# Optimization experiments

Hardware: AMD Instinct MI355X
Metric: run time of the kernel (lower is better)

Reference implementation:

```python
import jax, jax.numpy as jnp
import numpy as np

N_NODES = 50000
N_EDGES = 800000
B = 512
DIM_IN = 128
D2 = 200
D3 = 200
GC1 = 100
DG = 20
DH = 64
H1 = 128
H2 = 32
BN_EPS = 1e-5


def _lin_init(k, fan_in, fan_out):
    s = 1.0 / np.sqrt(fan_in)
    kw, kb = jax.random.split(k)
    W = jax.random.uniform(kw, (fan_in, fan_out), jnp.float32, -s, s)
    b = jax.random.uniform(kb, (fan_out,), jnp.float32, -s, s)
    return W, b


def setup_inputs() -> dict:
    key = jax.random.key(0)
    ks = jax.random.split(key, 16)
    feat = jax.random.normal(ks[0], (N_NODES, DIM_IN), jnp.float32)
    desc_2d = jax.random.normal(ks[1], (B, D2), jnp.float32)
    desc_3d = jax.random.normal(ks[2], (B, D3), jnp.float32)
    src = jax.random.randint(ks[3], (N_EDGES,), 0, N_NODES, jnp.int32)
    dst = jax.random.randint(ks[4], (N_EDGES,), 0, N_NODES, jnp.int32)
    graph_id = jnp.sort(jax.random.randint(ks[5], (N_NODES,), 0, B, jnp.int32))
    gc1_W, gc1_b = _lin_init(ks[6], DIM_IN, GC1)
    gc2_W, gc2_b = _lin_init(ks[7], GC1, DG)
    pg_W, pg_b = _lin_init(ks[8], DG, DH)
    p2_W, p2_b = _lin_init(ks[9], D2, DH)
    # xavier_uniform for W2
    lim = np.sqrt(6.0 / (DH + DH))
    W2 = jax.random.uniform(ks[10], (DH, DH), jnp.float32, -lim, lim)
    fusion_dim = (DG + 1) * (D2 + 1)
    fc1_W, fc1_b = _lin_init(ks[11], fusion_dim, H1)
    fc2_W, fc2_b = _lin_init(ks[12], H1, H2)
    fc3_W, fc3_b = _lin_init(ks[13], H2, 1)
    return {
        'feat': feat, 'desc_2d': desc_2d, 'desc_3d': desc_3d,
        'gc1_W': gc1_W, 'gc1_b': gc1_b, 'gc2_W': gc2_W, 'gc2_b': gc2_b,
        'pg_W': pg_W, 'pg_b': pg_b, 'p2_W': p2_W, 'p2_b': p2_b, 'W2': W2,
        'fc1_W': fc1_W, 'fc1_b': fc1_b, 'fc2_W': fc2_W, 'fc2_b': fc2_b,
        'fc3_W': fc3_W, 'fc3_b': fc3_b,
        'bn1_g': jnp.ones((H1,), jnp.float32), 'bn1_b': jnp.zeros((H1,), jnp.float32),
        'bn2_g': jnp.ones((H2,), jnp.float32), 'bn2_b': jnp.zeros((H2,), jnp.float32),
        'src': src, 'dst': dst, 'graph_id': graph_id,
    }


def _gcn(h, src, dst, W, b):
    # copy_u -> mean over incoming mailbox -> linear apply
    agg = jax.ops.segment_sum(h[src], dst, num_segments=N_NODES)
    deg = jax.ops.segment_sum(jnp.ones((src.shape[0],), h.dtype), dst, num_segments=N_NODES)
    h_mean = agg / jnp.maximum(deg, 1.0)[:, None]  # zero in-degree -> 0 (DGL default)
    return h_mean @ W + b


def _bn(x, g, b):
    mu = x.mean(0)
    var = x.var(0)
    return (x - mu) * jax.lax.rsqrt(var + BN_EPS) * g + b


def reference(feat, desc_2d, desc_3d, gc1_W, gc1_b, gc2_W, gc2_b,
              pg_W, pg_b, p2_W, p2_b, W2,
              fc1_W, fc1_b, fc2_W, fc2_b, fc3_W, fc3_b,
              bn1_g, bn1_b, bn2_g, bn2_b, src, dst, graph_id):
    h = jax.nn.relu(_gcn(feat, src, dst, gc1_W, gc1_b))          # [N, 100]
    h = jax.nn.relu(_gcn(h, src, dst, gc2_W, gc2_b))             # [N, 20]
    # dgl.mean_nodes: per-graph mean of node features
    cnt = jax.ops.segment_sum(jnp.ones((N_NODES,), h.dtype), graph_id, num_segments=B)
    hg = jax.ops.segment_sum(h, graph_id, num_segments=B) / jnp.maximum(cnt, 1.0)[:, None]  # [B, 20]
    h_g = hg @ pg_W + pg_b                                        # [B, 64]
    h_d = desc_2d @ p2_W + p2_b                                   # [B, 64]
    s = ((h_g @ W2) * h_d).sum(-1)                                # [B]
    a = jax.nn.sigmoid(s)[:, None]                                # [B, 1]
    ones = jnp.ones((B, 1), hg.dtype)
    hg1 = jnp.concatenate([hg, ones], axis=1)                     # [B, 21]
    d1 = jnp.concatenate([a * desc_2d, ones], axis=1)             # [B, 201]
    fusion = (hg1[:, :, None] * d1[:, None, :]).reshape(B, -1)    # [B, 21*201]
    out = jax.nn.relu(_bn(fusion @ fc1_W + fc1_b, bn1_g, bn1_b))
    out = jax.nn.relu(_bn(out @ fc2_W + fc2_b, bn2_g, bn2_b))
    return out @ fc3_W + fc3_b                                    # [B, 1]
```

## Files before the change

### kernel.cpp

```cpp
#include <hip/hip_runtime.h>

#define NN 50000
#define NE 800000
#define NB 512
#define DIN 128
#define DD2 200
#define C1 100
#define C2 20
#define DHH 64
#define HH1 128
#define HH2 32
#define KD 201
#define KDP 204
#define NU 2688
#define SCB 196
#define NCT 7
#define NTILE 3125
#define GB1 782
#define FPB 3125
#define FCB 672
#define PS1 128
#define SLOT 64
#define OVFCAP 8192

typedef short sh8 __attribute__((ext_vector_type(8)));
typedef float f32x4 __attribute__((ext_vector_type(4)));

__device__ __forceinline__ unsigned short f2bf(float x) {
    unsigned u = __float_as_uint(x);
    unsigned r = (u + 0x7fffu + ((u >> 16) & 1u)) >> 16;
    return (unsigned short)r;
}
__device__ __forceinline__ float bf_lo(unsigned u) { return __uint_as_float(u << 16); }
__device__ __forceinline__ float bf_hi(unsigned u) { return __uint_as_float(u & 0xffff0000u); }

__global__ void k_packB_init(const float* __restrict__ W, unsigned short* __restrict__ Bf,
                             int* __restrict__ cnt, float* __restrict__ hgs,
                             int* __restrict__ ovfc) {
    int idx = blockIdx.x * 256 + threadIdx.x;
    if (idx < NCT * 4 * 64) {
        int lane = idx & 63;
        int kc = (idx >> 6) & 3;
        int ct = idx >> 8;
        int col = ct * 16 + (lane & 15);
        int k0 = kc * 32 + (lane >> 4) * 8;
        unsigned short* outp = Bf + (size_t)idx * 8;
        #pragma unroll
        for (int e = 0; e < 8; ++e) {
            float v = (col < C1) ? W[(k0 + e) * C1 + col] : 0.f;
            outp[e] = f2bf(v);
        }
    }
    if (idx < NN) cnt[idx] = 0;
    if (idx < NB * C2) hgs[idx] = 0.f;
    if (idx == 0) *ovfc = 0;
}

__global__ __launch_bounds__(256) void k_front(const float* __restrict__ feat,
                                               const unsigned short* __restrict__ Bf,
                                               unsigned char* __restrict__ t1f8,
                                               const int* __restrict__ dst,
                                               int* __restrict__ cnt,
                                               int* __restrict__ pos,
                                               const float* __restrict__ desc2d,
                                               const float* __restrict__ W1,
                                               float* __restrict__ V) {
    __shared__ float smem[7168];
    const int tid = threadIdx.x;

    if (blockIdx.x >= GB1 && blockIdx.x < GB1 + FPB) {
        int e = (blockIdx.x - GB1) * 256 + tid;
        if (e < NE) pos[e] = atomicAdd(&cnt[dst[e]], 1);
        return;
    }

    if (blockIdx.x < GB1) {
        sh8* sB = (sh8*)smem;
        {
            const uint4* srcp = (const uint4*)Bf;
            uint4* dstp = (uint4*)smem;
            for (int i = tid; i < NCT * 4 * 64; i += 256) dstp[i] = srcp[i];
        }
        __syncthreads();
        const int w = tid >> 6, lane = tid & 63;
        const int ri = lane & 15;
        const int kg = lane >> 4;
        int tile = blockIdx.x * 4 + w;
        if (tile < NTILE) {
            const int n = tile * 16 + ri;
            f32x4 acc[NCT];
            #pragma unroll
            for (int ct = 0; ct < NCT; ++ct) acc[ct] = (f32x4){0.f, 0.f, 0.f, 0.f};
            #pragma unroll
            for (int kc = 0; kc < 4; ++kc) {
                const float* ap = feat + (size_t)n * DIN + kc * 32 + kg * 8;
                float4 a0 = *(const float4*)ap;
                float4 a1 = *(const float4*)(ap + 4);
                union { sh8 v; unsigned short u[8]; } af;
                af.u[0] = f2bf(a0.x); af.u[1] = f2bf(a0.y);
                af.u[2] = f2bf(a0.z); af.u[3] = f2bf(a0.w);
                af.u[4] = f2bf(a1.x); af.u[5] = f2bf(a1.y);
                af.u[6] = f2bf(a1.z); af.u[7] = f2bf(a1.w);
                #pragma unroll
                for (int ct = 0; ct < NCT; ++ct)
                    acc[ct] = __builtin_amdgcn_mfma_f32_16x16x32_bf16(
                        af.v, sB[(ct * 4 + kc) * 64 + lane], acc[ct], 0, 0, 0);
            }
            const int rbase = tile * 16 + kg * 4;
            #pragma unroll
            for (int ct = 0; ct < NCT; ++ct) {
                int col = ct * 16 + ri;
                if (col < C1) {
                    #pragma unroll
                    for (int r = 0; r < 4; ++r) {
                        int pk = __builtin_amdgcn_cvt_pk_fp8_f32(acc[ct][r], acc[ct][r], 0, false);
                        t1f8[(size_t)(rbase + r) * PS1 + col] = (unsigned char)(pk & 0xFF);
                    }
                }
            }
        }
        return;
    }

    {
        float (*S)[KDP] = (float(*)[KDP])smem;
        int fid = blockIdx.x - GB1 - FPB;
        const int i = fid / 32;
        const int rem = fid % 32;
        const int bt = rem >> 1;
        const int half = rem & 1;
        for (int idx = tid; idx < 32 * 50; idx += 256) {
            int r = idx / 50, c4 = idx % 50;
            *(float4*)&S[r][c4 * 4] =
                *(const float4*)(desc2d + (size_t)(bt * 32 + r) * DD2 + c4 * 4);
        }
        __syncthreads();
        const int c = tid & 31;
        const int rg = tid >> 5;
        float acc[4][2];
        #pragma unroll
        for (int r = 0; r < 4; ++r) { acc[r][0] = 0.f; acc[r][1] = 0.f; }
        const float* Wb = W1 + (size_t)i * (KD * HH1) + half * 64 + c;
        for (int k = 0; k < 200; k += 4) {
            const float* Wk = Wb + (size_t)k * HH1;
            float w0[2], w1[2], w2[2], w3[2];
            #pragma unroll
            for (int m = 0; m < 2; ++m) {
                w0[m] = Wk[32 * m];
                w1[m] = Wk[HH1 + 32 * m];
                w2[m] = Wk[2 * HH1 + 32 * m];
                w3[m] = Wk[3 * HH1 + 32 * m];
            }
            #pragma unroll
            for (int r = 0; r < 4; ++r) {
                float4 a4 = *(const float4*)&S[rg * 4 + r][k];
                #pragma unroll
                for (int m = 0; m < 2; ++m)
                    acc[r][m] += a4.x * w0[m] + a4.y * w1[m] + a4.z * w2[m] + a4.w * w3[m];
            }
        }
        #pragma unroll
        for (int r = 0; r < 4; ++r) {
            int b = bt * 32 + rg * 4 + r;
            float* Vr = V + (size_t)b * NU + i * HH1 + half * 64 + c;
            Vr[0] = acc[r][0];
            Vr[32] = acc[r][1];
        }
    }
}

__global__ void k_scat(const int* __restrict__ src, const int* __restrict__ dst,
                       const int* __restrict__ pos, int* __restrict__ epad,
                       int2* __restrict__ ovf, int* __restrict__ ovfc) {
    int e = blockIdx.x * 256 + threadIdx.x;
    if (e < NE) {
        int d = dst[e], p = pos[e], s = src[e];
        if (p < SLOT) {
            epad[(size_t)d * SLOT + p] = s;
        } else {
            int o = atomicAdd(ovfc, 1);
            if (o < OVFCAP) ovf[o] = make_int2(d, s);
        }
    }
}

__global__ __launch_bounds__(256) void k_agg1(const unsigned char* __restrict__ t1f8,
                                              const int* __restrict__ cnt,
                                              const int* __restrict__ epad,
                                              const int2* __restrict__ ovf,
                                              const int* __restrict__ ovfc,
                                              const float* __restrict__ b1,
                                              unsigned* __restrict__ h1b) {
    const int tid = threadIdx.x;
    const int w = tid >> 6, l = tid & 63;
    const int n = blockIdx.x * 4 + w;
    if (n >= NN || l >= 50) return;
    const int deg = cnt[n];
    const int m = deg < SLOT ? deg : SLOT;
    const int* ep = epad + (size_t)n * SLOT;
    const int co = 2 * l;
    float acc0 = 0.f, acc1 = 0.f;
    int e = 0;
    for (; e + 7 < m; e += 8) {
        int s0 = ep[e],     s1 = ep[e + 1], s2 = ep[e + 2], s3 = ep[e + 3];
        int s4 = ep[e + 4], s5 = ep[e + 5], s6 = ep[e + 6], s7 = ep[e + 7];
        int u0 = *(const unsigned short*)(t1f8 + (size_t)s0 * PS1 + co);
        int u1 = *(const unsigned short*)(t1f8 + (size_t)s1 * PS1 + co);
        int u2 = *(const unsigned short*)(t1f8 + (size_t)s2 * PS1 + co);
        int u3 = *(const unsigned short*)(t1f8 + (size_t)s3 * PS1 + co);
        int u4 = *(const unsigned short*)(t1f8 + (size_t)s4 * PS1 + co);
        int u5 = *(const unsigned short*)(t1f8 + (size_t)s5 * PS1 + co);
        int u6 = *(const unsigned short*)(t1f8 + (size_t)s6 * PS1 + co);
        int u7 = *(const unsigned short*)(t1f8 + (size_t)s7 * PS1 + co);
        acc0 += __builtin_amdgcn_cvt_f32_fp8(u0, 0); acc1 += __builtin_amdgcn_cvt_f32_fp8(u0, 1);
        acc0 += __builtin_amdgcn_cvt_f32_fp8(u1, 0); acc1 += __builtin_amdgcn_cvt_f32_fp8(u1, 1);
        acc0 += __builtin_amdgcn_cvt_f32_fp8(u2, 0); acc1 += __builtin_amdgcn_cvt_f32_fp8(u2, 1);
        acc0 += __builtin_amdgcn_cvt_f32_fp8(u3, 0); acc1 += __builtin_amdgcn_cvt_f32_fp8(u3, 1);
        acc0 += __builtin_amdgcn_cvt_f32_fp8(u4, 0); acc1 += __builtin_amdgcn_cvt_f32_fp8(u4, 1);
        acc0 += __builtin_amdgcn_cvt_f32_fp8(u5, 0); acc1 += __builtin_amdgcn_cvt_f32_fp8(u5, 1);
        acc0 += __builtin_amdgcn_cvt_f32_fp8(u6, 0); acc1 += __builtin_amdgcn_cvt_f32_fp8(u6, 1);
        acc0 += __builtin_amdgcn_cvt_f32_fp8(u7, 0); acc1 += __builtin_amdgcn_cvt_f32_fp8(u7, 1);
    }
    for (; e < m; ++e) {
        int u = *(const unsigned short*)(t1f8 + (size_t)ep[e] * PS1 + co);
        acc0 += __builtin_amdgcn_cvt_f32_fp8(u, 0);
        acc1 += __builtin_amdgcn_cvt_f32_fp8(u, 1);
    }
    if (deg > SLOT) {
        int novf = *ovfc; novf = novf < OVFCAP ? novf : OVFCAP;
        for (int j2 = 0; j2 < novf; ++j2) {
            int2 p = ovf[j2];
            if (p.x == n) {
                int u = *(const unsigned short*)(t1f8 + (size_t)p.y * PS1 + co);
                acc0 += __builtin_amdgcn_cvt_f32_fp8(u, 0);
                acc1 += __builtin_amdgcn_cvt_f32_fp8(u, 1);
            }
        }
    }
    float d = (float)(deg > 0 ? deg : 1);
    float v0 = fmaxf(acc0 / d + b1[co], 0.f);
    float v1 = fmaxf(acc1 / d + b1[co + 1], 0.f);
    h1b[(size_t)n * 50 + l] = (unsigned)f2bf(v0) | ((unsigned)f2bf(v1) << 16);
}

__global__ void k_gemm2(const unsigned* __restrict__ h1b, const float* __restrict__ W,
                        unsigned* __restrict__ t2b) {
    __shared__ float sW[C1 * C2];
    __shared__ float sr[16][C1];
    __shared__ float sc[16][C2];
    for (int idx = threadIdx.x; idx < C1 * C2; idx += 320) sW[idx] = W[idx];
    int ln = threadIdx.x / C2, j = threadIdx.x % C2;
    int n0 = blockIdx.x * 16;
    for (int idx = threadIdx.x; idx < 16 * 50; idx += 320) {
        int r = idx / 50, c = idx % 50;
        int n = n0 + r;
        unsigned u = (n < NN) ? h1b[(size_t)n * 50 + c] : 0u;
        sr[r][2 * c] = bf_lo(u);
        sr[r][2 * c + 1] = bf_hi(u);
    }
    __syncthreads();
    if (ln < 16) {
        float acc = 0.f;
        #pragma unroll 4
        for (int k = 0; k < C1; ++k) acc += sr[ln][k] * sW[k * C2 + j];
        sc[ln][j] = acc;
    }
    __syncthreads();
    for (int idx = threadIdx.x; idx < 16 * 10; idx += 320) {
        int r = idx / 10, jp = idx % 10;
        int n = n0 + r;
        if (n < NN)
            t2b[(size_t)n * 10 + jp] =
                (unsigned)f2bf(sc[r][2 * jp]) | ((unsigned)f2bf(sc[r][2 * jp + 1]) << 16);
    }
}

__global__ void k_agg2p(const unsigned* __restrict__ t2b, const int* __restrict__ cnt,
                        const int* __restrict__ epad, const int2* __restrict__ ovf,
                        const int* __restrict__ ovfc, const float* __restrict__ bias,
                        const int* __restrict__ gid, float* __restrict__ hgs) {
    int ln = threadIdx.x / C2, c = threadIdx.x % C2;
    if (ln >= 12) return;
    int n = blockIdx.x * 12 + ln;
    if (n >= NN) return;
    const int deg = cnt[n];
    const int m = deg < SLOT ? deg : SLOT;
    const int* ep = epad + (size_t)n * SLOT;
    const int jp = c >> 1, hi = c & 1;
    float acc = 0.f;
    int e = 0;
    for (; e + 3 < m; e += 4) {
        int s0 = ep[e], s1 = ep[e + 1], s2 = ep[e + 2], s3 = ep[e + 3];
        unsigned u0 = t2b[(size_t)s0 * 10 + jp];
        unsigned u1 = t2b[(size_t)s1 * 10 + jp];
        unsigned u2 = t2b[(size_t)s2 * 10 + jp];
        unsigned u3 = t2b[(size_t)s3 * 10 + jp];
        acc += hi ? bf_hi(u0) : bf_lo(u0);
        acc += hi ? bf_hi(u1) : bf_lo(u1);
        acc += hi ? bf_hi(u2) : bf_lo(u2);
        acc += hi ? bf_hi(u3) : bf_lo(u3);
    }
    for (; e < m; ++e) {
        unsigned u = t2b[(size_t)ep[e] * 10 + jp];
        acc += hi ? bf_hi(u) : bf_lo(u);
    }
    if (deg > SLOT) {
        int novf = *ovfc; novf = novf < OVFCAP ? novf : OVFCAP;
        for (int j2 = 0; j2 < novf; ++j2) {
            int2 p = ovf[j2];
            if (p.x == n) {
                unsigned u = t2b[(size_t)p.y * 10 + jp];
                acc += hi ? bf_hi(u) : bf_lo(u);
            }
        }
    }
    float d = (float)(deg > 0 ? deg : 1);
    float v = acc / d + bias[c];
    v = v > 0.f ? v : 0.f;
    atomicAdd(&hgs[gid[n] * C2 + c], v);
}

__global__ __launch_bounds__(128) void k_hfc1(const float* __restrict__ hgs,
                                              const int* __restrict__ gid,
                                              const float* __restrict__ desc2d,
                                              const float* __restrict__ pgW,
                                              const float* __restrict__ pgb,
                                              const float* __restrict__ p2W,
                                              const float* __restrict__ p2b,
                                              const float* __restrict__ W2,
                                              const float* __restrict__ V,
                                              const float* __restrict__ W1,
                                              float* __restrict__ o1) {
    __shared__ float shg[C2];
    __shared__ float sg[DHH];
    __shared__ float sa;
    const int b = blockIdx.x, tid = threadIdx.x;
    if (tid < C2) {
        int lo = 0, hi = NN;
        while (lo < hi) { int m = (lo + hi) >> 1; if (gid[m] < b) lo = m + 1; else hi = m; }
        int lo2 = lo, hi2 = NN;
        while (lo2 < hi2) { int m = (lo2 + hi2) >> 1; if (gid[m] < b + 1) lo2 = m + 1; else hi2 = m; }
        float dcnt = (float)(lo2 - lo);
        if (dcnt < 1.f) dcnt = 1.f;
        shg[tid] = hgs[b * C2 + tid] / dcnt;
    }
    __syncthreads();
    float hdj = 0.f;
    if (tid < DHH) {
        float hgj = pgb[tid];
        #pragma unroll
        for (int k = 0; k < C2; ++k) hgj += shg[k] * pgW[k * DHH + tid];
        hdj = p2b[tid];
        #pragma unroll 4
        for (int k = 0; k < DD2; ++k) hdj += desc2d[b * DD2 + k] * p2W[k * DHH + tid];
        sg[tid] = hgj;
    }
    __syncthreads();
    if (tid < DHH) {
        float tj = 0.f;
        #pragma unroll 4
        for (int k = 0; k < DHH; ++k) tj += sg[k] * W2[k * DHH + tid];
        float v = tj * hdj;
        #pragma unroll
        for (int off = 32; off; off >>= 1) v += __shfl_xor(v, off, 64);
        if (tid == 0) sa = 1.f / (1.f + expf(-v));
    }
    __syncthreads();
    const int j = tid;
    const float* Vb = V + (size_t)b * NU + j;
    const float* WL = W1 + (size_t)200 * HH1 + j;
    float sv = Vb[20 * HH1];
    float sw = WL[(size_t)20 * KD * HH1];
    #pragma unroll
    for (int i = 0; i < 20; ++i) {
        float h = shg[i];
        sv += h * Vb[i * HH1];
        sw += h * WL[(size_t)i * KD * HH1];
    }
    o1[b * HH1 + j] = sa * sv + sw;
}

__global__ __launch_bounds__(128) void k_fc2s(const float* __restrict__ o1,
                                              const float* __restrict__ g,
                                              const float* __restrict__ beta,
                                              const float* __restrict__ W,
                                              float* __restrict__ o2) {
    __shared__ float r[HH1];
    __shared__ float part[4][HH2];
    const int tid = threadIdx.x;
    float s = 0.f, s2 = 0.f;
    for (int b = 0; b < NB; ++b) {
        float v = o1[b * HH1 + tid];
        s += v; s2 += v * v;
    }
    float mu = s / NB;
    float rstd = rsqrtf(s2 / NB - mu * mu + 1e-5f);
    float scale = rstd * g[tid];
    float shift = beta[tid] - mu * scale;
    const int m = tid & 31, p = tid >> 5;
    for (int q = 0; q < 4; ++q) {
        int b = blockIdx.x * 4 + q;
        float v = o1[b * HH1 + tid];
        __syncthreads();
        r[tid] = fmaxf(v * scale + shift, 0.f);
        __syncthreads();
        float acc = 0.f;
        #pragma unroll 4
        for (int j = p * 32; j < p * 32 + 32; ++j) acc += r[j] * W[j * HH2 + m];
        part[p][m] = acc;
        __syncthreads();
        if (tid < HH2) o2[b * HH2 + tid] = part[0][tid] + part[1][tid] + part[2][tid] + part[3][tid];
    }
}

__global__ __launch_bounds__(512) void k_finals(const float* __restrict__ o2,
                                                const float* __restrict__ g,
                                                const float* __restrict__ beta,
                                                const float* __restrict__ W3,
                                                const float* __restrict__ b3,
                                                float* __restrict__ out) {
    __shared__ float ps[16][HH2], ps2[16][HH2];
    __shared__ float sscale[HH2], sshift[HH2];
    const int tid = threadIdx.x;
    const int gq = tid >> 5, m = tid & 31;
    float s = 0.f, s2 = 0.f;
    for (int rr = 0; rr < 32; ++rr) {
        float v = o2[(gq * 32 + rr) * HH2 + m];
        s += v; s2 += v * v;
    }
    ps[gq][m] = s; ps2[gq][m] = s2;
    __syncthreads();
    if (tid < HH2) {
        float ts = 0.f, ts2 = 0.f;
        #pragma unroll
        for (int q = 0; q < 16; ++q) { ts += ps[q][tid]; ts2 += ps2[q][tid]; }
        float mu = ts / NB;
        float rstd = rsqrtf(ts2 / NB - mu * mu + 1e-5f);
        float scale = rstd * g[tid];
        sscale[tid] = scale;
        sshift[tid] = beta[tid] - mu * scale;
    }
    __syncthreads();
    float acc = b3[0];
    #pragma unroll 4
    for (int mm = 0; mm < HH2; ++mm) {
        float v = o2[tid * HH2 + mm];
        acc += fmaxf(v * sscale[mm] + sshift[mm], 0.f) * W3[mm];
    }
    out[tid] = acc;
}

extern "C" void kernel_launch(void* const* d_in, const int* in_sizes, int n_in,
                              void* d_out, int out_size, void* d_ws, size_t ws_size,
                              hipStream_t stream) {
    const float* feat   = (const float*)d_in[0];
    const float* desc2d = (const float*)d_in[1];
    const float* gc1W = (const float*)d_in[3];
    const float* gc1b = (const float*)d_in[4];
    const float* gc2W = (const float*)d_in[5];
    const float* gc2b = (const float*)d_in[6];
    const float* pgW  = (const float*)d_in[7];
    const float* pgb  = (const float*)d_in[8];
    const float* p2W  = (const float*)d_in[9];
    const float* p2b  = (const float*)d_in[10];
    const float* W2   = (const float*)d_in[11];
    const float* fc1W = (const float*)d_in[12];
    const float* fc2W = (const float*)d_in[14];
    const float* fc3W = (const float*)d_in[16];
    const float* fc3b = (const float*)d_in[17];
    const float* bn1g = (const float*)d_in[18];
    const float* bn1b = (const float*)d_in[19];
    const float* bn2g = (const float*)d_in[20];
    const float* bn2b = (const float*)d_in[21];
    const int* src = (const int*)d_in[22];
    const int* dst = (const int*)d_in[23];
    const int* gid = (const int*)d_in[24];
    float* out = (float*)d_out;

    char* ws = (char*)d_ws;
    size_t off = 0;
    auto alloc = [&](size_t nb) {
        void* p = ws + off;
        off = (off + nb + 255) & ~(size_t)255;
        return p;
    };
    unsigned char* t1f8 = (unsigned char*)alloc((size_t)NN * PS1);
    unsigned* h1b = (unsigned*)alloc((size_t)NN * 50 * 4);
    unsigned* t2b = (unsigned*)alloc((size_t)NN * 10 * 4);
    int* cnt_in  = (int*)alloc((size_t)NN * 4);
    int* pos     = (int*)alloc((size_t)NE * 4);
    int* epad    = (int*)alloc((size_t)NN * SLOT * 4);
    int2* ovf    = (int2*)alloc((size_t)OVFCAP * 8);
    int* ovfc    = (int*)alloc(256);
    unsigned short* Bf = (unsigned short*)alloc((size_t)NCT * 4 * 64 * 16);
    float* V     = (float*)alloc((size_t)NB * NU * 4);
    float* hgs   = (float*)alloc((size_t)NB * C2 * 4);
    float* o1    = (float*)alloc((size_t)NB * HH1 * 4);
    float* o2    = (float*)alloc((size_t)NB * HH2 * 4);

    k_packB_init<<<SCB, 256, 0, stream>>>(gc1W, Bf, cnt_in, hgs, ovfc);
    k_front<<<GB1 + FPB + FCB, 256, 0, stream>>>(feat, Bf, t1f8, dst, cnt_in, pos,
                                                 desc2d, fc1W, V);
    k_scat<<<(NE + 255) / 256, 256, 0, stream>>>(src, dst, pos, epad, ovf, ovfc);

    k_agg1<<<(NN + 3) / 4, 256, 0, stream>>>(t1f8, cnt_in, epad, ovf, ovfc, gc1b, h1b);
    k_gemm2<<<(NN + 15) / 16, 320, 0, stream>>>(h1b, gc2W, t2b);
    k_agg2p<<<(NN + 11) / 12, 256, 0, stream>>>(t2b, cnt_in, epad, ovf, ovfc, gc2b, gid, hgs);

    k_hfc1<<<NB, 128, 0, stream>>>(hgs, gid, desc2d, pgW, pgb, p2W, p2b, W2, V, fc1W, o1);
    k_fc2s<<<NB / 4, 128, 0, stream>>>(o1, bn1g, bn1b, fc2W, o2);
    k_finals<<<1, 512, 0, stream>>>(o2, bn2g, bn2b, fc3W, fc3b, out);
}
```

Before: 194.3 us.

## Fuse all stages into one persistent cooperative kernel with grid syncs

Replaces the nine separate kernel launches with a single cooperative persistent kernel that loops over work items and uses grid-wide syncs between stages. The MFMA GEMM, fc1 precompute and degree counting are interleaved in one job loop. The goal is to remove launch overhead and inter-kernel gaps. In exchange, the grid is capped at occupancy-limited size (at most 2048 blocks), which may reduce per-stage parallelism and adds grid-sync costs. Register pressure is also higher because every stage shares one kernel body.

```diff
diff --git a/kernel.cpp b/kernel.cpp
--- a/kernel.cpp
+++ b/kernel.cpp
@@ -1,4 +1,7 @@
 #include <hip/hip_runtime.h>
+#include <hip/hip_cooperative_groups.h>
+
+namespace cg = cooperative_groups;
 
 #define NN 50000
 #define NE 800000
@@ -13,12 +16,12 @@
 #define KD 201
 #define KDP 204
 #define NU 2688
-#define SCB 196
 #define NCT 7
 #define NTILE 3125
 #define GB1 782
+#define FCB 672
 #define FPB 3125
-#define FCB 672
+#define J2 4688
 #define PS1 128
 #define SLOT 64
 #define OVFCAP 8192
@@ -34,480 +37,487 @@
 __device__ __forceinline__ float bf_lo(unsigned u) { return __uint_as_float(u << 16); }
 __device__ __forceinline__ float bf_hi(unsigned u) { return __uint_as_float(u & 0xffff0000u); }
 
-__global__ void k_packB_init(const float* __restrict__ W, unsigned short* __restrict__ Bf,
-                             int* __restrict__ cnt, float* __restrict__ hgs,
-                             int* __restrict__ ovfc) {
-    int idx = blockIdx.x * 256 + threadIdx.x;
-    if (idx < NCT * 4 * 64) {
-        int lane = idx & 63;
-        int kc = (idx >> 6) & 3;
-        int ct = idx >> 8;
-        int col = ct * 16 + (lane & 15);
-        int k0 = kc * 32 + (lane >> 4) * 8;
-        unsigned short* outp = Bf + (size_t)idx * 8;
-        #pragma unroll
-        for (int e = 0; e < 8; ++e) {
-            float v = (col < C1) ? W[(k0 + e) * C1 + col] : 0.f;
-            outp[e] = f2bf(v);
-        }
-    }
-    if (idx < NN) cnt[idx] = 0;
-    if (idx < NB * C2) hgs[idx] = 0.f;
-    if (idx == 0) *ovfc = 0;
-}
-
-__global__ __launch_bounds__(256) void k_front(const float* __restrict__ feat,
-                                               const unsigned short* __restrict__ Bf,
-                                               unsigned char* __restrict__ t1f8,
-                                               const int* __restrict__ dst,
-                                               int* __restrict__ cnt,
-                                               int* __restrict__ pos,
-                                               const float* __restrict__ desc2d,
-                                               const float* __restrict__ W1,
-                                               float* __restrict__ V) {
-    __shared__ float smem[7168];
+struct Params {
+    const float* feat; const float* desc2d;
+    const float* gc1W; const float* gc1b; const float* gc2W; const float* gc2b;
+    const float* pgW; const float* pgb; const float* p2W; const float* p2b;
+    const float* W2; const float* fc1W; const float* fc2W;
+    const float* fc3W; const float* fc3b;
+    const float* bn1g; const float* bn1b; const float* bn2g; const float* bn2b;
+    const int* src; const int* dst; const int* gid;
+    unsigned char* t1f8; unsigned* h1b; unsigned* t2b;
+    int* cnt; int* pos; int* epad; int2* ovf; int* ovfc;
+    unsigned short* Bf; float* V; float* hgs; float* o1; float* o2;
+    float* out;
+};
+
+__global__ __launch_bounds__(256, 4) void k_mega(Params p) {
+    __shared__ __align__(16) char smem[28672];
+    cg::grid_group grid = cg::this_grid();
     const int tid = threadIdx.x;
-
-    if (blockIdx.x >= GB1 && blockIdx.x < GB1 + FPB) {
-        int e = (blockIdx.x - GB1) * 256 + tid;
-        if (e < NE) pos[e] = atomicAdd(&cnt[dst[e]], 1);
-        return;
-    }
-
-    if (blockIdx.x < GB1) {
-        sh8* sB = (sh8*)smem;
-        {
-            const uint4* srcp = (const uint4*)Bf;
-            uint4* dstp = (uint4*)smem;
-            for (int i = tid; i < NCT * 4 * 64; i += 256) dstp[i] = srcp[i];
-        }
-        __syncthreads();
-        const int w = tid >> 6, lane = tid & 63;
-        const int ri = lane & 15;
-        const int kg = lane >> 4;
-        int tile = blockIdx.x * 4 + w;
-        if (tile < NTILE) {
-            const int n = tile * 16 + ri;
-            f32x4 acc[NCT];
-            #pragma unroll
-            for (int ct = 0; ct < NCT; ++ct) acc[ct] = (f32x4){0.f, 0.f, 0.f, 0.f};
-            #pragma unroll
-            for (int kc = 0; kc < 4; ++kc) {
-                const float* ap = feat + (size_t)n * DIN + kc * 32 + kg * 8;
-                float4 a0 = *(const float4*)ap;
-                float4 a1 = *(const float4*)(ap + 4);
-                union { sh8 v; unsigned short u[8]; } af;
-                af.u[0] = f2bf(a0.x); af.u[1] = f2bf(a0.y);
-                af.u[2] = f2bf(a0.z); af.u[3] = f2bf(a0.w);
-                af.u[4] = f2bf(a1.x); af.u[5] = f2bf(a1.y);
-                af.u[6] = f2bf(a1.z); af.u[7] = f2bf(a1.w);
+    const int bid = blockIdx.x;
+    const int gdim = gridDim.x;
+
+    {
+        const int gt = bid * 256 + tid, gs = gdim * 256;
+        for (int i = gt; i < NN; i += gs) {
+            p.cnt[i] = 0;
+            if (i < NCT * 4 * 64) {
+                int lane = i & 63, kc = (i >> 6) & 3, ct = i >> 8;
+                int col = ct * 16 + (lane & 15);
+                int k0 = kc * 32 + (lane >> 4) * 8;
+                unsigned short* outp = p.Bf + (size_t)i * 8;
                 #pragma unroll
-                for (int ct = 0; ct < NCT; ++ct)
-                    acc[ct] = __builtin_amdgcn_mfma_f32_16x16x32_bf16(
-                        af.v, sB[(ct * 4 + kc) * 64 + lane], acc[ct], 0, 0, 0);
-            }
-            const int rbase = tile * 16 + kg * 4;
-            #pragma unroll
-            for (int ct = 0; ct < NCT; ++ct) {
-                int col = ct * 16 + ri;
-                if (col < C1) {
+                for (int e = 0; e < 8; ++e) {
+                    float v = (col < C1) ? p.gc1W[(k0 + e) * C1 + col] : 0.f;
+                    outp[e] = f2bf(v);
+                }
+            }
+            if (i < NB * C2) p.hgs[i] = 0.f;
+            if (i == 0) *p.ovfc = 0;
+        }
+    }
+    grid.sync();
+
+    {
+        int lstate = -1;
+        for (int j = bid; j < J2; j += gdim) {
+            if (j % 3 == 0) {
+                int cj = j / 3;
+                if (cj < GB1) {
+                    sh8* sB = (sh8*)smem;
+                    if (lstate != 0) {
+                        __syncthreads();
+                        const uint4* srcp = (const uint4*)p.Bf;
+                        uint4* dstp = (uint4*)smem;
+                        for (int i = tid; i < NCT * 4 * 64; i += 256) dstp[i] = srcp[i];
+                        lstate = 0;
+                    }
+                    __syncthreads();
+                    const int w = tid >> 6, lane = tid & 63;
+                    const int ri = lane & 15, kg = lane >> 4;
+                    int tile = cj * 4 + w;
+                    if (tile < NTILE) {
+                        const int n = tile * 16 + ri;
+                        f32x4 acc[NCT];
+                        #pragma unroll
+                        for (int ct = 0; ct < NCT; ++ct) acc[ct] = (f32x4){0.f, 0.f, 0.f, 0.f};
+                        #pragma unroll
+                        for (int kc = 0; kc < 4; ++kc) {
+                            const float* ap = p.feat + (size_t)n * DIN + kc * 32 + kg * 8;
+                            float4 a0 = *(const float4*)ap;
+                            float4 a1 = *(const float4*)(ap + 4);
+                            union { sh8 v; unsigned short u[8]; } af;
+                            af.u[0] = f2bf(a0.x); af.u[1] = f2bf(a0.y);
+                            af.u[2] = f2bf(a0.z); af.u[3] = f2bf(a0.w);
+                            af.u[4] = f2bf(a1.x); af.u[5] = f2bf(a1.y);
+                            af.u[6] = f2bf(a1.z); af.u[7] = f2bf(a1.w);
+                            #pragma unroll
+                            for (int ct = 0; ct < NCT; ++ct)
+                                acc[ct] = __builtin_amdgcn_mfma_f32_16x16x32_bf16(
+                                    af.v, sB[(ct * 4 + kc) * 64 + lane], acc[ct], 0, 0, 0);
+                        }
+                        const int rbase = tile * 16 + kg * 4;
+                        #pragma unroll
+                        for (int ct = 0; ct < NCT; ++ct) {
+                            int col = ct * 16 + ri;
+                            if (col < C1) {
+                                #pragma unroll
+                                for (int r = 0; r < 4; ++r) {
+                                    int pk = __builtin_amdgcn_cvt_pk_fp8_f32(acc[ct][r], acc[ct][r], 0, false);
+                                    p.t1f8[(size_t)(rbase + r) * PS1 + col] = (unsigned char)(pk & 0xFF);
+                                }
+                            }
+                        }
+                    }
+                } else if (cj < GB1 + FCB) {
+                    int fid = cj - GB1;
+                    float (*S)[KDP] = (float(*)[KDP])smem;
+                    const int i = fid / 32;
+                    const int rem = fid % 32;
+                    const int bt = rem >> 1, half = rem & 1;
+                    __syncthreads();
+                    for (int idx = tid; idx < 32 * 50; idx += 256) {
+                        int r = idx / 50, c4 = idx % 50;
+                        *(float4*)&S[r][c4 * 4] =
+                            *(const float4*)(p.desc2d + (size_t)(bt * 32 + r) * DD2 + c4 * 4);
+                    }
+                    __syncthreads();
+                    const int c = tid & 31, rg = tid >> 5;
+                    float acc[4][2];
+                    #pragma unroll
+                    for (int r = 0; r < 4; ++r) { acc[r][0] = 0.f; acc[r][1] = 0.f; }
+                    const float* Wb = p.fc1W + (size_t)i * (KD * HH1) + half * 64 + c;
+                    for (int k = 0; k < 200; k += 4) {
+                        const float* Wk = Wb + (size_t)k * HH1;
+                        float w0[2], w1[2], w2[2], w3[2];
+                        #pragma unroll
+                        for (int m = 0; m < 2; ++m) {
+                            w0[m] = Wk[32 * m];
+                            w1[m] = Wk[HH1 + 32 * m];
+                            w2[m] = Wk[2 * HH1 + 32 * m];
+                            w3[m] = Wk[3 * HH1 + 32 * m];
+                        }
+                        #pragma unroll
+                        for (int r = 0; r < 4; ++r) {
+                            float4 a4 = *(const float4*)&S[rg * 4 + r][k];
+                            #pragma unroll
+                            for (int m = 0; m < 2; ++m)
+                                acc[r][m] += a4.x * w0[m] + a4.y * w1[m] + a4.z * w2[m] + a4.w * w3[m];
+                        }
+                    }
                     #pragma unroll
                     for (int r = 0; r < 4; ++r) {
-                        int pk = __builtin_amdgcn_cvt_pk_fp8_f32(acc[ct][r], acc[ct][r], 0, false);
-                        t1f8[(size_t)(rbase + r) * PS1 + col] = (unsigned char)(pk & 0xFF);
-                    }
-                }
-            }
-        }
-        return;
-    }
-
-    {
-        float (*S)[KDP] = (float(*)[KDP])smem;
-        int fid = blockIdx.x - GB1 - FPB;
-        const int i = fid / 32;
-        const int rem = fid % 32;
-        const int bt = rem >> 1;
-        const int half = rem & 1;
-        for (int idx = tid; idx < 32 * 50; idx += 256) {
-            int r = idx / 50, c4 = idx % 50;
-            *(float4*)&S[r][c4 * 4] =
-                *(const float4*)(desc2d + (size_t)(bt * 32 + r) * DD2 + c4 * 4);
-        }
-        __syncthreads();
-        const int c = tid & 31;
-        const int rg = tid >> 5;
-        float acc[4][2];
-        #pragma unroll
-        for (int r = 0; r < 4; ++r) { acc[r][0] = 0.f; acc[r][1] = 0.f; }
-        const float* Wb = W1 + (size_t)i * (KD * HH1) + half * 64 + c;
-        for (int k = 0; k < 200; k += 4) {
-            const float* Wk = Wb + (size_t)k * HH1;
-            float w0[2], w1[2], w2[2], w3[2];
-            #pragma unroll
-            for (int m = 0; m < 2; ++m) {
-                w0[m] = Wk[32 * m];
-                w1[m] = Wk[HH1 + 32 * m];
-                w2[m] = Wk[2 * HH1 + 32 * m];
-                w3[m] = Wk[3 * HH1 + 32 * m];
-            }
-            #pragma unroll
-            for (int r = 0; r < 4; ++r) {
-                float4 a4 = *(const float4*)&S[rg * 4 + r][k];
-                #pragma unroll
-                for (int m = 0; m < 2; ++m)
-                    acc[r][m] += a4.x * w0[m] + a4.y * w1[m] + a4.z * w2[m] + a4.w * w3[m];
-            }
-        }
-        #pragma unroll
-        for (int r = 0; r < 4; ++r) {
-            int b = bt * 32 + rg * 4 + r;
-            float* Vr = V + (size_t)b * NU + i * HH1 + half * 64 + c;
-            Vr[0] = acc[r][0];
-            Vr[32] = acc[r][1];
-        }
-    }
-}
-
-__global__ void k_scat(const int* __restrict__ src, const int* __restrict__ dst,
-                       const int* __restrict__ pos, int* __restrict__ epad,
-                       int2* __restrict__ ovf, int* __restrict__ ovfc) {
-    int e = blockIdx.x * 256 + threadIdx.x;
-    if (e < NE) {
-        int d = dst[e], p = pos[e], s = src[e];
-        if (p < SLOT) {
-            epad[(size_t)d * SLOT + p] = s;
-        } else {
-            int o = atomicAdd(ovfc, 1);
-            if (o < OVFCAP) ovf[o] = make_int2(d, s);
-        }
-    }
-}
-
-__global__ __launch_bounds__(256) void k_agg1(const unsigned char* __restrict__ t1f8,
-                                              const int* __restrict__ cnt,
-                                              const int* __restrict__ epad,
-                                              const int2* __restrict__ ovf,
-                                              const int* __restrict__ ovfc,
-                                              const float* __restrict__ b1,
-                                              unsigned* __restrict__ h1b) {
-    const int tid = threadIdx.x;
-    const int w = tid >> 6, l = tid & 63;
-    const int n = blockIdx.x * 4 + w;
-    if (n >= NN || l >= 50) return;
-    const int deg = cnt[n];
-    const int m = deg < SLOT ? deg : SLOT;
-    const int* ep = epad + (size_t)n * SLOT;
-    const int co = 2 * l;
-    float acc0 = 0.f, acc1 = 0.f;
-    int e = 0;
-    for (; e + 7 < m; e += 8) {
-        int s0 = ep[e],     s1 = ep[e + 1], s2 = ep[e + 2], s3 = ep[e + 3];
-        int s4 = ep[e + 4], s5 = ep[e + 5], s6 = ep[e + 6], s7 = ep[e + 7];
-        int u0 = *(const unsigned short*)(t1f8 + (size_t)s0 * PS1 + co);
-        int u1 = *(const unsigned short*)(t1f8 + (size_t)s1 * PS1 + co);
-        int u2 = *(const unsigned short*)(t1f8 + (size_t)s2 * PS1 + co);
-        int u3 = *(const unsigned short*)(t1f8 + (size_t)s3 * PS1 + co);
-        int u4 = *(const unsigned short*)(t1f8 + (size_t)s4 * PS1 + co);
-        int u5 = *(const unsigned short*)(t1f8 + (size_t)s5 * PS1 + co);
-        int u6 = *(const unsigned short*)(t1f8 + (size_t)s6 * PS1 + co);
-        int u7 = *(const unsigned short*)(t1f8 + (size_t)s7 * PS1 + co);
-        acc0 += __builtin_amdgcn_cvt_f32_fp8(u0, 0); acc1 += __builtin_amdgcn_cvt_f32_fp8(u0, 1);
-        acc0 += __builtin_amdgcn_cvt_f32_fp8(u1, 0); acc1 += __builtin_amdgcn_cvt_f32_fp8(u1, 1);
-        acc0 += __builtin_amdgcn_cvt_f32_fp8(u2, 0); acc1 += __builtin_amdgcn_cvt_f32_fp8(u2, 1);
-        acc0 += __builtin_amdgcn_cvt_f32_fp8(u3, 0); acc1 += __builtin_amdgcn_cvt_f32_fp8(u3, 1);
-        acc0 += __builtin_amdgcn_cvt_f32_fp8(u4, 0); acc1 += __builtin_amdgcn_cvt_f32_fp8(u4, 1);
-        acc0 += __builtin_amdgcn_cvt_f32_fp8(u5, 0); acc1 += __builtin_amdgcn_cvt_f32_fp8(u5, 1);
-        acc0 += __builtin_amdgcn_cvt_f32_fp8(u6, 0); acc1 += __builtin_amdgcn_cvt_f32_fp8(u6, 1);
-        acc0 += __builtin_amdgcn_cvt_f32_fp8(u7, 0); acc1 += __builtin_amdgcn_cvt_f32_fp8(u7, 1);
-    }
-    for (; e < m; ++e) {
-        int u = *(const unsigned short*)(t1f8 + (size_t)ep[e] * PS1 + co);
-        acc0 += __builtin_amdgcn_cvt_f32_fp8(u, 0);
-        acc1 += __builtin_amdgcn_cvt_f32_fp8(u, 1);
-    }
-    if (deg > SLOT) {
-        int novf = *ovfc; novf = novf < OVFCAP ? novf : OVFCAP;
-        for (int j2 = 0; j2 < novf; ++j2) {
-            int2 p = ovf[j2];
-            if (p.x == n) {
-                int u = *(const unsigned short*)(t1f8 + (size_t)p.y * PS1 + co);
+                        int b = bt * 32 + rg * 4 + r;
+                        float* Vr = p.V + (size_t)b * NU + i * HH1 + half * 64 + c;
+                        Vr[0] = acc[r][0];
+                        Vr[32] = acc[r][1];
+                    }
+                    lstate = 1;
+                }
+            } else {
+                int fj = j - j / 3 - 1;
+                if (fj < FPB) {
+                    int e = fj * 256 + tid;
+                    if (e < NE) p.pos[e] = atomicAdd(&p.cnt[p.dst[e]], 1);
+                }
+            }
+        }
+    }
+    grid.sync();
+
+    for (int job = bid; job < FPB; job += gdim) {
+        int e = job * 256 + tid;
+        if (e < NE) {
+            int d = p.dst[e], pp = p.pos[e], s = p.src[e];
+            if (pp < SLOT) {
+                p.epad[(size_t)d * SLOT + pp] = s;
+            } else {
+                int o = atomicAdd(p.ovfc, 1);
+                if (o < OVFCAP) p.ovf[o] = make_int2(d, s);
+            }
+        }
+    }
+    grid.sync();
+
+    for (int job = bid; job < 12500; job += gdim) {
+        const int w = tid >> 6, l = tid & 63;
+        const int n = job * 4 + w;
+        if (n < NN && l < 50) {
+            const int deg = p.cnt[n];
+            const int m = deg < SLOT ? deg : SLOT;
+            const int* ep = p.epad + (size_t)n * SLOT;
+            const int co = 2 * l;
+            float acc0 = 0.f, acc1 = 0.f;
+            int e = 0;
+            for (; e + 7 < m; e += 8) {
+                int s0 = ep[e],     s1 = ep[e + 1], s2 = ep[e + 2], s3 = ep[e + 3];
+                int s4 = ep[e + 4], s5 = ep[e + 5], s6 = ep[e + 6], s7 = ep[e + 7];
+                int u0 = *(const unsigned short*)(p.t1f8 + (size_t)s0 * PS1 + co);
+                int u1 = *(const unsigned short*)(p.t1f8 + (size_t)s1 * PS1 + co);
+                int u2 = *(const unsigned short*)(p.t1f8 + (size_t)s2 * PS1 + co);
+                int u3 = *(const unsigned short*)(p.t1f8 + (size_t)s3 * PS1 + co);
+                int u4 = *(const unsigned short*)(p.t1f8 + (size_t)s4 * PS1 + co);
+                int u5 = *(const unsigned short*)(p.t1f8 + (size_t)s5 * PS1 + co);
+                int u6 = *(const unsigned short*)(p.t1f8 + (size_t)s6 * PS1 + co);
+                int u7 = *(const unsigned short*)(p.t1f8 + (size_t)s7 * PS1 + co);
+                acc0 += __builtin_amdgcn_cvt_f32_fp8(u0, 0); acc1 += __builtin_amdgcn_cvt_f32_fp8(u0, 1);
+                acc0 += __builtin_amdgcn_cvt_f32_fp8(u1, 0); acc1 += __builtin_amdgcn_cvt_f32_fp8(u1, 1);
+                acc0 += __builtin_amdgcn_cvt_f32_fp8(u2, 0); acc1 += __builtin_amdgcn_cvt_f32_fp8(u2, 1);
+                acc0 += __builtin_amdgcn_cvt_f32_fp8(u3, 0); acc1 += __builtin_amdgcn_cvt_f32_fp8(u3, 1);
+                acc0 += __builtin_amdgcn_cvt_f32_fp8(u4, 0); acc1 += __builtin_amdgcn_cvt_f32_fp8(u4, 1);
+                acc0 += __builtin_amdgcn_cvt_f32_fp8(u5, 0); acc1 += __builtin_amdgcn_cvt_f32_fp8(u5, 1);
+                acc0 += __builtin_amdgcn_cvt_f32_fp8(u6, 0); acc1 += __builtin_amdgcn_cvt_f32_fp8(u6, 1);
+                acc0 += __builtin_amdgcn_cvt_f32_fp8(u7, 0); acc1 += __builtin_amdgcn_cvt_f32_fp8(u7, 1);
+            }
+            for (; e < m; ++e) {
+                int u = *(const unsigned short*)(p.t1f8 + (size_t)ep[e] * PS1 + co);
                 acc0 += __builtin_amdgcn_cvt_f32_fp8(u, 0);
                 acc1 += __builtin_amdgcn_cvt_f32_fp8(u, 1);
             }
-        }
-    }
-    float d = (float)(deg > 0 ? deg : 1);
-    float v0 = fmaxf(acc0 / d + b1[co], 0.f);
-    float v1 = fmaxf(acc1 / d + b1[co + 1], 0.f);
-    h1b[(size_t)n * 50 + l] = (unsigned)f2bf(v0) | ((unsigned)f2bf(v1) << 16);
-}
-
-__global__ void k_gemm2(const unsigned* __restrict__ h1b, const float* __restrict__ W,
-                        unsigned* __restrict__ t2b) {
-    __shared__ float sW[C1 * C2];
-    __shared__ float sr[16][C1];
-    __shared__ float sc[16][C2];
-    for (int idx = threadIdx.x; idx < C1 * C2; idx += 320) sW[idx] = W[idx];
-    int ln = threadIdx.x / C2, j = threadIdx.x % C2;
-    int n0 = blockIdx.x * 16;
-    for (int idx = threadIdx.x; idx < 16 * 50; idx += 320) {
-        int r = idx / 50, c = idx % 50;
-        int n = n0 + r;
-        unsigned u = (n < NN) ? h1b[(size_t)n * 50 + c] : 0u;
-        sr[r][2 * c] = bf_lo(u);
-        sr[r][2 * c + 1] = bf_hi(u);
-    }
-    __syncthreads();
-    if (ln < 16) {
-        float acc = 0.f;
-        #pragma unroll 4
-        for (int k = 0; k < C1; ++k) acc += sr[ln][k] * sW[k * C2 + j];
-        sc[ln][j] = acc;
-    }
-    __syncthreads();
-    for (int idx = threadIdx.x; idx < 16 * 10; idx += 320) {
-        int r = idx / 10, jp = idx % 10;
-        int n = n0 + r;
-        if (n < NN)
-            t2b[(size_t)n * 10 + jp] =
-                (unsigned)f2bf(sc[r][2 * jp]) | ((unsigned)f2bf(sc[r][2 * jp + 1]) << 16);
-    }
-}
-
-__global__ void k_agg2p(const unsigned* __restrict__ t2b, const int* __restrict__ cnt,
-                        const int* __restrict__ epad, const int2* __restrict__ ovf,
-                        const int* __restrict__ ovfc, const float* __restrict__ bias,
-                        const int* __restrict__ gid, float* __restrict__ hgs) {
-    int ln = threadIdx.x / C2, c = threadIdx.x % C2;
-    if (ln >= 12) return;
-    int n = blockIdx.x * 12 + ln;
-    if (n >= NN) return;
-    const int deg = cnt[n];
-    const int m = deg < SLOT ? deg : SLOT;
-    const int* ep = epad + (size_t)n * SLOT;
-    const int jp = c >> 1, hi = c & 1;
-    float acc = 0.f;
-    int e = 0;
-    for (; e + 3 < m; e += 4) {
-        int s0 = ep[e], s1 = ep[e + 1], s2 = ep[e + 2], s3 = ep[e + 3];
-        unsigned u0 = t2b[(size_t)s0 * 10 + jp];
-        unsigned u1 = t2b[(size_t)s1 * 10 + jp];
-        unsigned u2 = t2b[(size_t)s2 * 10 + jp];
-        unsigned u3 = t2b[(size_t)s3 * 10 + jp];
-        acc += hi ? bf_hi(u0) : bf_lo(u0);
-        acc += hi ? bf_hi(u1) : bf_lo(u1);
-        acc += hi ? bf_hi(u2) : bf_lo(u2);
-        acc += hi ? bf_hi(u3) : bf_lo(u3);
-    }
-    for (; e < m; ++e) {
-        unsigned u = t2b[(size_t)ep[e] * 10 + jp];
-        acc += hi ? bf_hi(u) : bf_lo(u);
-    }
-    if (deg > SLOT) {
-        int novf = *ovfc; novf = novf < OVFCAP ? novf : OVFCAP;
-        for (int j2 = 0; j2 < novf; ++j2) {
-            int2 p = ovf[j2];
-            if (p.x == n) {
-                unsigned u = t2b[(size_t)p.y * 10 + jp];
-                acc += hi ? bf_hi(u) : bf_lo(u);
-            }
-        }
-    }
-    float d = (float)(deg > 0 ? deg : 1);
-    float v = acc / d + bias[c];
-    v = v > 0.f ? v : 0.f;
-    atomicAdd(&hgs[gid[n] * C2 + c], v);
-}
-
-__global__ __launch_bounds__(128) void k_hfc1(const float* __restrict__ hgs,
-                                              const int* __restrict__ gid,
-                                              const float* __restrict__ desc2d,
-                                              const float* __restrict__ pgW,
-                                              const float* __restrict__ pgb,
-                                              const float* __restrict__ p2W,
-                                              const float* __restrict__ p2b,
-                                              const float* __restrict__ W2,
-                                              const float* __restrict__ V,
-                                              const float* __restrict__ W1,
-                                              float* __restrict__ o1) {
-    __shared__ float shg[C2];
-    __shared__ float sg[DHH];
-    __shared__ float sa;
-    const int b = blockIdx.x, tid = threadIdx.x;
-    if (tid < C2) {
-        int lo = 0, hi = NN;
-        while (lo < hi) { int m = (lo + hi) >> 1; if (gid[m] < b) lo = m + 1; else hi = m; }
-        int lo2 = lo, hi2 = NN;
-        while (lo2 < hi2) { int m = (lo2 + hi2) >> 1; if (gid[m] < b + 1) lo2 = m + 1; else hi2 = m; }
-        float dcnt = (float)(lo2 - lo);
-        if (dcnt < 1.f) dcnt = 1.f;
-        shg[tid] = hgs[b * C2 + tid] / dcnt;
-    }
-    __syncthreads();
-    float hdj = 0.f;
-    if (tid < DHH) {
-        float hgj = pgb[tid];
-        #pragma unroll
-        for (int k = 0; k < C2; ++k) hgj += shg[k] * pgW[k * DHH + tid];
-        hdj = p2b[tid];
-        #pragma unroll 4
-        for (int k = 0; k < DD2; ++k) hdj += desc2d[b * DD2 + k] * p2W[k * DHH + tid];
-        sg[tid] = hgj;
-    }
-    __syncthreads();
-    if (tid < DHH) {
-        float tj = 0.f;
-        #pragma unroll 4
-        for (int k = 0; k < DHH; ++k) tj += sg[k] * W2[k * DHH + tid];
-        float v = tj * hdj;
-        #pragma unroll
-        for (int off = 32; off; off >>= 1) v += __shfl_xor(v, off, 64);
-        if (tid == 0) sa = 1.f / (1.f + expf(-v));
-    }
-    __syncthreads();
-    const int j = tid;
-    const float* Vb = V + (size_t)b * NU + j;
-    const float* WL = W1 + (size_t)200 * HH1 + j;
-    float sv = Vb[20 * HH1];
-    float sw = WL[(size_t)20 * KD * HH1];
-    #pragma unroll
-    for (int i = 0; i < 20; ++i) {
-        float h = shg[i];
-        sv += h * Vb[i * HH1];
-        sw += h * WL[(size_t)i * KD * HH1];
-    }
-    o1[b * HH1 + j] = sa * sv + sw;
-}
-
-__global__ __launch_bounds__(128) void k_fc2s(const float* __restrict__ o1,
-                                              const float* __restrict__ g,
-                                              const float* __restrict__ beta,
-                                              const float* __restrict__ W,
-                                              float* __restrict__ o2) {
-    __shared__ float r[HH1];
-    __shared__ float part[4][HH2];
-    const int tid = threadIdx.x;
-    float s = 0.f, s2 = 0.f;
-    for (int b = 0; b < NB; ++b) {
-        float v = o1[b * HH1 + tid];
-        s += v; s2 += v * v;
-    }
-    float mu = s / NB;
-    float rstd = rsqrtf(s2 / NB - mu * mu + 1e-5f);
-    float scale = rstd * g[tid];
-    float shift = beta[tid] - mu * scale;
-    const int m = tid & 31, p = tid >> 5;
-    for (int q = 0; q < 4; ++q) {
-        int b = blockIdx.x * 4 + q;
-        float v = o1[b * HH1 + tid];
+            if (deg > SLOT) {
+                int novf = *p.ovfc; novf = novf < OVFCAP ? novf : OVFCAP;
+                for (int j2 = 0; j2 < novf; ++j2) {
+                    int2 pr = p.ovf[j2];
+                    if (pr.x == n) {
+                        int u = *(const unsigned short*)(p.t1f8 + (size_t)pr.y * PS1 + co);
+                        acc0 += __builtin_amdgcn_cvt_f32_fp8(u, 0);
+                        acc1 += __builtin_amdgcn_cvt_f32_fp8(u, 1);
+                    }
+                }
+            }
+            float d = (float)(deg > 0 ? deg : 1);
+            float v0 = fmaxf(acc0 / d + p.gc1b[co], 0.f);
+            float v1 = fmaxf(acc1 / d + p.gc1b[co + 1], 0.f);
+            p.h1b[(size_t)n * 50 + l] = (unsigned)f2bf(v0) | ((unsigned)f2bf(v1) << 16);
+        }
+    }
+    grid.sync();
+
+    {
+        float* sW = (float*)smem;
+        float (*sr)[C1] = (float(*)[C1])(smem + 8192);
+        float (*sc)[C2] = (float(*)[C2])(smem + 13312);
         __syncthreads();
-        r[tid] = fmaxf(v * scale + shift, 0.f);
+        for (int idx = tid; idx < C1 * C2; idx += 256) sW[idx] = p.gc2W[idx];
+        for (int job = bid; job < 4167; job += gdim) {
+            __syncthreads();
+            int n0 = job * 12;
+            for (int idx = tid; idx < 12 * 50; idx += 256) {
+                int r = idx / 50, c = idx % 50;
+                int n = n0 + r;
+                unsigned u = (n < NN) ? p.h1b[(size_t)n * 50 + c] : 0u;
+                sr[r][2 * c] = bf_lo(u);
+                sr[r][2 * c + 1] = bf_hi(u);
+            }
+            __syncthreads();
+            int ln = tid / C2, j = tid % C2;
+            if (ln < 12) {
+                float acc = 0.f;
+                #pragma unroll 4
+                for (int k = 0; k < C1; ++k) acc += sr[ln][k] * sW[k * C2 + j];
+                sc[ln][j] = acc;
+            }
+            __syncthreads();
+            for (int idx = tid; idx < 12 * 10; idx += 256) {
+                int r = idx / 10, jp = idx % 10;
+                int n = n0 + r;
+                if (n < NN)
+                    p.t2b[(size_t)n * 10 + jp] =
+                        (unsigned)f2bf(sc[r][2 * jp]) | ((unsigned)f2bf(sc[r][2 * jp + 1]) << 16);
+            }
+        }
+    }
+    grid.sync();
+
+    for (int job = bid; job < 4167; job += gdim) {
+        int ln = tid / C2, c = tid % C2;
+        if (ln < 12) {
+            int n = job * 12 + ln;
+            if (n < NN) {
+                const int deg = p.cnt[n];
+                const int m = deg < SLOT ? deg : SLOT;
+                const int* ep = p.epad + (size_t)n * SLOT;
+                const int jp = c >> 1, hi = c & 1;
+                float acc = 0.f;
+                int e = 0;
+                for (; e + 3 < m; e += 4) {
+                    int s0 = ep[e], s1 = ep[e + 1], s2 = ep[e + 2], s3 = ep[e + 3];
+                    unsigned u0 = p.t2b[(size_t)s0 * 10 + jp];
+                    unsigned u1 = p.t2b[(size_t)s1 * 10 + jp];
+                    unsigned u2 = p.t2b[(size_t)s2 * 10 + jp];
+                    unsigned u3 = p.t2b[(size_t)s3 * 10 + jp];
+                    acc += hi ? bf_hi(u0) : bf_lo(u0);
+                    acc += hi ? bf_hi(u1) : bf_lo(u1);
+                    acc += hi ? bf_hi(u2) : bf_lo(u2);
+                    acc += hi ? bf_hi(u3) : bf_lo(u3);
+                }
+                for (; e < m; ++e) {
+                    unsigned u = p.t2b[(size_t)ep[e] * 10 + jp];
+                    acc += hi ? bf_hi(u) : bf_lo(u);
+                }
+                if (deg > SLOT) {
+                    int novf = *p.ovfc; novf = novf < OVFCAP ? novf : OVFCAP;
+                    for (int j2 = 0; j2 < novf; ++j2) {
+                        int2 pr = p.ovf[j2];
+                        if (pr.x == n) {
+                            unsigned u = p.t2b[(size_t)pr.y * 10 + jp];
+                            acc += hi ? bf_hi(u) : bf_lo(u);
+                        }
+                    }
+                }
+                float d = (float)(deg > 0 ? deg : 1);
+                float v = fmaxf(acc / d + p.gc2b[c], 0.f);
+                atomicAdd(&p.hgs[p.gid[n] * C2 + c], v);
+            }
+        }
+    }
+    grid.sync();
+
+    {
+        float* shg = (float*)smem;
+        float* sg  = shg + 2 * C2;
+        float* sa  = sg + 2 * DHH;
+        for (int job = bid; job < NB / 2; job += gdim) {
+            __syncthreads();
+            const int w = tid >> 7, t2 = tid & 127;
+            const int b = job * 2 + w;
+            if (t2 < C2) {
+                int lo = 0, hi = NN;
+                while (lo < hi) { int m = (lo + hi) >> 1; if (p.gid[m] < b) lo = m + 1; else hi = m; }
+                int lo2 = lo, hi2 = NN;
+                while (lo2 < hi2) { int m = (lo2 + hi2) >> 1; if (p.gid[m] < b + 1) lo2 = m + 1; else hi2 = m; }
+                float dcnt = (float)(lo2 - lo);
+                if (dcnt < 1.f) dcnt = 1.f;
+                shg[w * C2 + t2] = p.hgs[b * C2 + t2] / dcnt;
+            }
+            __syncthreads();
+            float hdj = 0.f;
+            if (t2 < DHH) {
+                float hgj = p.pgb[t2];
+                #pragma unroll
+                for (int k = 0; k < C2; ++k) hgj += shg[w * C2 + k] * p.pgW[k * DHH + t2];
+                hdj = p.p2b[t2];
+                #pragma unroll 4
+                for (int k = 0; k < DD2; ++k) hdj += p.desc2d[b * DD2 + k] * p.p2W[k * DHH + t2];
+                sg[w * DHH + t2] = hgj;
+            }
+            __syncthreads();
+            if (t2 < DHH) {
+                float tj = 0.f;
+                #pragma unroll 4
+                for (int k = 0; k < DHH; ++k) tj += sg[w * DHH + k] * p.W2[k * DHH + t2];
+                float v = tj * hdj;
+                #pragma unroll
+                for (int off = 32; off; off >>= 1) v += __shfl_xor(v, off, 64);
+                if (t2 == 0) sa[w] = 1.f / (1.f + expf(-v));
+            }
+            __syncthreads();
+            const float* Vb = p.V + (size_t)b * NU + t2;
+            const float* WL = p.fc1W + (size_t)200 * HH1 + t2;
+            float sv = Vb[20 * HH1];
+            float sw = WL[(size_t)20 * KD * HH1];
+            #pragma unroll
+            for (int i = 0; i < 20; ++i) {
+                float h = shg[w * C2 + i];
+                sv += h * Vb[i * HH1];
+                sw += h * WL[(size_t)i * KD * HH1];
+            }
+            p.o1[b * HH1 + t2] = sa[w] * sv + sw;
+        }
+    }
+    grid.sync();
+
+    {
+        float* rbuf = (float*)smem;
+        float* part = rbuf + 128;
+        for (int job = bid; job < 128; job += gdim) {
+            float scale = 0.f, shift = 0.f;
+            if (tid < HH1) {
+                float s = 0.f, s2 = 0.f;
+                for (int b = 0; b < NB; ++b) {
+                    float v = p.o1[b * HH1 + tid];
+                    s += v; s2 += v * v;
+                }
+                float mu = s / NB;
+                float rstd = rsqrtf(s2 / NB - mu * mu + 1e-5f);
+                scale = rstd * p.bn1g[tid];
+                shift = p.bn1b[tid] - mu * scale;
+            }
+            const int m = tid & 31, pq = (tid >> 5) & 3;
+            for (int q = 0; q < 4; ++q) {
+                int b = job * 4 + q;
+                float v = (tid < HH1) ? p.o1[b * HH1 + tid] : 0.f;
+                __syncthreads();
+                if (tid < HH1) rbuf[tid] = fmaxf(v * scale + shift, 0.f);
+                __syncthreads();
+                if (tid < HH1) {
+                    float acc = 0.f;
+                    #pragma unroll 4
+                    for (int j = pq * 32; j < pq * 32 + 32; ++j) acc += rbuf[j] * p.fc2W[j * HH2 + m];
+                    part[pq * 32 + m] = acc;
+                }
+                __syncthreads();
+                if (tid < HH2)
+                    p.o2[b * HH2 + tid] = part[tid] + part[32 + tid] + part[64 + tid] + part[96 + tid];
+                __syncthreads();
+            }
+        }
+    }
+    grid.sync();
+
+    if (bid == 0) {
+        float* ps  = (float*)smem;
+        float* ps2 = ps + 256;
+        float* sscale = ps2 + 256;
+        float* sshift = sscale + 32;
+        const int gq = tid >> 5, m = tid & 31;
+        float s = 0.f, s2 = 0.f;
+        for (int rr = 0; rr < 64; ++rr) {
+            float v = p.o2[(gq * 64 + rr) * HH2 + m];
+            s += v; s2 += v * v;
+        }
+        ps[gq * 32 + m] = s; ps2[gq * 32 + m] = s2;
         __syncthreads();
-        float acc = 0.f;
-        #pragma unroll 4
-        for (int j = p * 32; j < p * 32 + 32; ++j) acc += r[j] * W[j * HH2 + m];
-        part[p][m] = acc;
+        if (tid < HH2) {
+            float ts = 0.f, ts2 = 0.f;
+            #pragma unroll
+            for (int q = 0; q < 8; ++q) { ts += ps[q * 32 + tid]; ts2 += ps2[q * 32 + tid]; }
+            float mu = ts / NB;
+            float rstd = rsqrtf(ts2 / NB - mu * mu + 1e-5f);
+            float scale = rstd * p.bn2g[tid];
+            sscale[tid] = scale;
+            sshift[tid] = p.bn2b[tid] - mu * scale;
+        }
         __syncthreads();
-        if (tid < HH2) o2[b * HH2 + tid] = part[0][tid] + part[1][tid] + part[2][tid] + part[3][tid];
-    }
-}
-
-__global__ __launch_bounds__(512) void k_finals(const float* __restrict__ o2,
-                                                const float* __restrict__ g,
-                                                const float* __restrict__ beta,
-                                                const float* __restrict__ W3,
-                                                const float* __restrict__ b3,
-                                                float* __restrict__ out) {
-    __shared__ float ps[16][HH2], ps2[16][HH2];
-    __shared__ float sscale[HH2], sshift[HH2];
-    const int tid = threadIdx.x;
-    const int gq = tid >> 5, m = tid & 31;
-    float s = 0.f, s2 = 0.f;
-    for (int rr = 0; rr < 32; ++rr) {
-        float v = o2[(gq * 32 + rr) * HH2 + m];
-        s += v; s2 += v * v;
-    }
-    ps[gq][m] = s; ps2[gq][m] = s2;
-    __syncthreads();
-    if (tid < HH2) {
-        float ts = 0.f, ts2 = 0.f;
-        #pragma unroll
-        for (int q = 0; q < 16; ++q) { ts += ps[q][tid]; ts2 += ps2[q][tid]; }
-        float mu = ts / NB;
-        float rstd = rsqrtf(ts2 / NB - mu * mu + 1e-5f);
-        float scale = rstd * g[tid];
-        sscale[tid] = scale;
-        sshift[tid] = beta[tid] - mu * scale;
-    }
-    __syncthreads();
-    float acc = b3[0];
-    #pragma unroll 4
-    for (int mm = 0; mm < HH2; ++mm) {
-        float v = o2[tid * HH2 + mm];
-        acc += fmaxf(v * sscale[mm] + sshift[mm], 0.f) * W3[mm];
-    }
-    out[tid] = acc;
+        for (int b = tid; b < NB; b += 256) {
+            float acc = p.fc3b[0];
+            #pragma unroll 4
+            for (int mm = 0; mm < HH2; ++mm) {
+                float v = p.o2[b * HH2 + mm];
+                acc += fmaxf(v * sscale[mm] + sshift[mm], 0.f) * p.fc3W[mm];
+            }
+            p.out[b] = acc;
+        }
+    }
 }
 
 extern "C" void kernel_launch(void* const* d_in, const int* in_sizes, int n_in,
                               void* d_out, int out_size, void* d_ws, size_t ws_size,
                               hipStream_t stream) {
-    const float* feat   = (const float*)d_in[0];
-    const float* desc2d = (const float*)d_in[1];
-    const float* gc1W = (const float*)d_in[3];
-    const float* gc1b = (const float*)d_in[4];
-    const float* gc2W = (const float*)d_in[5];
-    const float* gc2b = (const float*)d_in[6];
-    const float* pgW  = (const float*)d_in[7];
-    const float* pgb  = (const float*)d_in[8];
-    const float* p2W  = (const float*)d_in[9];
-    const float* p2b  = (const float*)d_in[10];
-    const float* W2   = (const float*)d_in[11];
-    const float* fc1W = (const float*)d_in[12];
-    const float* fc2W = (const float*)d_in[14];
-    const float* fc3W = (const float*)d_in[16];
-    const float* fc3b = (const float*)d_in[17];
-    const float* bn1g = (const float*)d_in[18];
-    const float* bn1b = (const float*)d_in[19];
-    const float* bn2g = (const float*)d_in[20];
-    const float* bn2b = (const float*)d_in[21];
-    const int* src = (const int*)d_in[22];
-    const int* dst = (const int*)d_in[23];
-    const int* gid = (const int*)d_in[24];
-    float* out = (float*)d_out;
-
     char* ws = (char*)d_ws;
     size_t off = 0;
     auto alloc = [&](size_t nb) {
-        void* p = ws + off;
+        void* pp = ws + off;
         off = (off + nb + 255) & ~(size_t)255;
-        return p;
+        return pp;
     };
-    unsigned char* t1f8 = (unsigned char*)alloc((size_t)NN * PS1);
-    unsigned* h1b = (unsigned*)alloc((size_t)NN * 50 * 4);
-    unsigned* t2b = (unsigned*)alloc((size_t)NN * 10 * 4);
-    int* cnt_in  = (int*)alloc((size_t)NN * 4);
-    int* pos     = (int*)alloc((size_t)NE * 4);
-    int* epad    = (int*)alloc((size_t)NN * SLOT * 4);
-    int2* ovf    = (int2*)alloc((size_t)OVFCAP * 8);
-    int* ovfc    = (int*)alloc(256);
-    unsigned short* Bf = (unsigned short*)alloc((size_t)NCT * 4 * 64 * 16);
-    float* V     = (float*)alloc((size_t)NB * NU * 4);
-    float* hgs   = (float*)alloc((size_t)NB * C2 * 4);
-    float* o1    = (float*)alloc((size_t)NB * HH1 * 4);
-    float* o2    = (float*)alloc((size_t)NB * HH2 * 4);
-
-    k_packB_init<<<SCB, 256, 0, stream>>>(gc1W, Bf, cnt_in, hgs, ovfc);
-    k_front<<<GB1 + FPB + FCB, 256, 0, stream>>>(feat, Bf, t1f8, dst, cnt_in, pos,
-                                                 desc2d, fc1W, V);
-    k_scat<<<(NE + 255) / 256, 256, 0, stream>>>(src, dst, pos, epad, ovf, ovfc);
-
-    k_agg1<<<(NN + 3) / 4, 256, 0, stream>>>(t1f8, cnt_in, epad, ovf, ovfc, gc1b, h1b);
-    k_gemm2<<<(NN + 15) / 16, 320, 0, stream>>>(h1b, gc2W, t2b);
-    k_agg2p<<<(NN + 11) / 12, 256, 0, stream>>>(t2b, cnt_in, epad, ovf, ovfc, gc2b, gid, hgs);
-
-    k_hfc1<<<NB, 128, 0, stream>>>(hgs, gid, desc2d, pgW, pgb, p2W, p2b, W2, V, fc1W, o1);
-    k_fc2s<<<NB / 4, 128, 0, stream>>>(o1, bn1g, bn1b, fc2W, o2);
-    k_finals<<<1, 512, 0, stream>>>(o2, bn2g, bn2b, fc3W, fc3b, out);
+    Params p;
+    p.feat   = (const float*)d_in[0];
+    p.desc2d = (const float*)d_in[1];
+    p.gc1W = (const float*)d_in[3];
+    p.gc1b = (const float*)d_in[4];
+    p.gc2W = (const float*)d_in[5];
+    p.gc2b = (const float*)d_in[6];
+    p.pgW  = (const float*)d_in[7];
+    p.pgb  = (const float*)d_in[8];
+    p.p2W  = (const float*)d_in[9];
+    p.p2b  = (const float*)d_in[10];
+    p.W2   = (const float*)d_in[11];
+    p.fc1W = (const float*)d_in[12];
+    p.fc2W = (const float*)d_in[14];
+    p.fc3W = (const float*)d_in[16];
+    p.fc3b = (const float*)d_in[17];
+    p.bn1g = (const float*)d_in[18];
+    p.bn1b = (const float*)d_in[19];
+    p.bn2g = (const float*)d_in[20];
+    p.bn2b = (const float*)d_in[21];
+    p.src = (const int*)d_in[22];
+    p.dst = (const int*)d_in[23];
+    p.gid = (const int*)d_in[24];
+    p.out = (float*)d_out;
+
+    p.t1f8 = (unsigned char*)alloc((size_t)NN * PS1);
+    p.h1b  = (unsigned*)alloc((size_t)NN * 50 * 4);
+    p.t2b  = (unsigned*)alloc((size_t)NN * 10 * 4);
+    p.cnt  = (int*)alloc((size_t)NN * 4);
+    p.pos  = (int*)alloc((size_t)NE * 4);
+    p.epad = (int*)alloc((size_t)NN * SLOT * 4);
+    p.ovf  = (int2*)alloc((size_t)OVFCAP * 8);
+    p.ovfc = (int*)alloc(256);
+    p.Bf   = (unsigned short*)alloc((size_t)NCT * 4 * 64 * 16);
+    p.V    = (float*)alloc((size_t)NB * NU * 4);
+    p.hgs  = (float*)alloc((size_t)NB * C2 * 4);
+    p.o1   = (float*)alloc((size_t)NB * HH1 * 4);
+    p.o2   = (float*)alloc((size_t)NB * HH2 * 4);
+
+    int maxb = 0;
+    hipOccupancyMaxActiveBlocksPerMultiprocessor(&maxb, k_mega, 256, 0);
+    if (maxb < 1) maxb = 1;
+    long long grid = (long long)maxb * 256;
+    if (grid > 2048) grid = 2048;
+
+    void* args[] = { (void*)&p };
+    hipLaunchCooperativeKernel((void*)k_mega, dim3((unsigned)grid), dim3(256),
+                               args, 0, stream);
 }
```

After: 742.3 us. +282.0%, slower.
